# Performance work log

Hardware: AMD Instinct MI355X
Metric: run time of the kernel (lower is better)

## Reference

```python
import jax, jax.numpy as jnp
import numpy as np

B, N, D_IN = 8, 1369, 768
S, D, ITERS = 7, 256, 3
RES, SIGMA = 37, 5.0
EPS = 1e-8


def _ln(x, g, b):
    m = jnp.mean(x, -1, keepdims=True)
    v = jnp.mean((x - m) ** 2, -1, keepdims=True)
    return (x - m) * jax.lax.rsqrt(v + 1e-5) * g + b


def _abs_grid():
    xs = jnp.linspace(-1.0, 1.0, RES)
    ys = jnp.linspace(-1.0, 1.0, RES)
    gx, gy = jnp.meshgrid(xs, ys, indexing='xy')
    return jnp.stack([gx.reshape(-1), gy.reshape(-1)], axis=-1)  # [N,2]


def setup_inputs() -> dict:
    key = jax.random.key(0)
    ks = jax.random.split(key, 40)
    i = iter(range(40))
    def w(shape, scale=0.02):
        return (jax.random.normal(ks[next(i)], shape, jnp.float32) * scale).astype(jnp.float32)
    def zeros(shape):
        return jnp.zeros(shape, jnp.float32)
    xav = float(np.sqrt(6.0 / (S + D)))
    inp = {
        'inputs': jax.random.normal(ks[next(i)], (B, N, D_IN), jnp.float32),
        'slots_init_p': jax.random.uniform(ks[next(i)], (1, S, D), jnp.float32, -xav, xav),
        'S_s0': w((1, S, 1, 2)),
        'S_p0': w((1, S, 1, 2)),
        'im_ln1_g': jnp.ones((D_IN,), jnp.float32), 'im_ln1_b': zeros((D_IN,)),
        'im_w1': w((D_IN, D_IN)), 'im_b1': zeros((D_IN,)),
        'im_w2': w((D_IN, D)), 'im_b2': zeros((D,)),
        'im_ln2_g': jnp.ones((D,), jnp.float32), 'im_ln2_b': zeros((D,)),
        'Wq': w((D, D)), 'Wk': w((D, D)), 'Wv': w((D, D)),
        'g_w': w((2, D)), 'g_b': zeros((D,)),
        'f_w1': w((D, D)), 'f_b1': zeros((D,)),
        'f_w2': w((D, D)), 'f_b2': zeros((D,)),
        'ln_g': jnp.ones((D,), jnp.float32), 'ln_b': zeros((D,)),
        'gru_wih': w((D, 3 * D)), 'gru_whh': w((D, 3 * D)),
        'gru_bih': zeros((3 * D,)), 'gru_bhh': zeros((3 * D,)),
        'mlp_ln_g': jnp.ones((D,), jnp.float32), 'mlp_ln_b': zeros((D,)),
        'mlp_w1': w((D, 4 * D)), 'mlp_b1': zeros((4 * D,)),
        'mlp_w2': w((4 * D, D)), 'mlp_b2': zeros((D,)),
        'fin_w': w((D, D)), 'fin_b': zeros((D,)),
    }
    return inp


def reference(inputs, slots_init_p, S_s0, S_p0,
              im_ln1_g, im_ln1_b, im_w1, im_b1, im_w2, im_b2, im_ln2_g, im_ln2_b,
              Wq, Wk, Wv, g_w, g_b, f_w1, f_b1, f_w2, f_b2,
              ln_g, ln_b, gru_wih, gru_whh, gru_bih, gru_bhh,
              mlp_ln_g, mlp_ln_b, mlp_w1, mlp_b1, mlp_w2, mlp_b2,
              fin_w, fin_b):
    abs_grid = _abs_grid()                    # [N,2], constant buffer
    ag = abs_grid[None, None]                 # [1,1,N,2]
    scale = D ** (-0.5)

    slots = jnp.broadcast_to(slots_init_p, (B, S, D))
    slots_init = slots

    # initial_mlp: LN -> Linear -> ReLU -> Linear -> LN (dropout-free eval path)
    x = _ln(inputs, im_ln1_g, im_ln1_b)
    x = jax.nn.relu(x @ im_w1 + im_b1)
    x = x @ im_w2 + im_b2
    x = _ln(x, im_ln2_g, im_ln2_b)            # [B,N,D]
    KX = x @ Wk                                # slot-independent part of K(inputs)
    VX = x @ Wv

    S_p = jnp.broadcast_to(S_p0, (B, S, 1, 2))
    S_s = jnp.broadcast_to(S_s0, (B, S, 1, 2))

    def f_mlp(z):
        return jax.nn.relu(z @ f_w1 + f_b1) @ f_w2 + f_b2

    attn = None
    slots_prev = slots
    for t in range(ITERS + 1):
        if t == ITERS - 1:  # query_opt straight-through trick
            slots = jax.lax.stop_gradient(slots) + slots_init - jax.lax.stop_gradient(slots_init)
        slots_prev = slots
        sn = _ln(slots, ln_g, ln_b)
        rel = (ag - S_p) / (S_s * SIGMA)      # [B,S,N,2]
        grel = rel @ g_w + g_b                # [B,S,N,D]
        k = f_mlp(KX[:, None] + grel)         # [B,S,N,D]
        v = f_mlp(VX[:, None] + grel)
        q = sn @ Wq                           # [B,S,D]
        dots = jnp.einsum('bsd,bsnd->bsn', q, k) * scale
        attn = jax.nn.softmax(dots, axis=1) + EPS   # softmax over slots
        attn = attn / jnp.sum(attn, -1, keepdims=True)
        updates = jnp.einsum('bsnd,bsn->bsd', v, attn)
        S_p = jnp.einsum('bsn,nd->bsd', attn, abs_grid)[:, :, None, :]
        S_s = jnp.sqrt(jnp.einsum('bsnd,bsn->bsd', (ag - S_p) ** 2, attn))[:, :, None, :]
        if t != ITERS:
            # GRUCell (torch gate order r,z,n)
            gi = updates @ gru_wih + gru_bih
            gh = slots_prev @ gru_whh + gru_bhh
            i_r, i_z, i_n = jnp.split(gi, 3, axis=-1)
            h_r, h_z, h_n = jnp.split(gh, 3, axis=-1)
            r = jax.nn.sigmoid(i_r + h_r)
            z = jax.nn.sigmoid(i_z + h_z)
            n = jnp.tanh(i_n + r * h_n)
            slots = (1.0 - z) * n + z * slots_prev
            # residual pre-norm MLP (dropout identity in eval)
            m = _ln(slots, mlp_ln_g, mlp_ln_b)
            m = jax.nn.relu(m @ mlp_w1 + mlp_b1) @ mlp_w2 + mlp_b2
            slots = slots + m
    out = slots_prev @ fin_w + fin_b
    return out, attn
```

## Files before the change

kernel.cpp:

```cpp
#include <hip/hip_runtime.h>

constexpr int CB   = 8;
constexpr int CN   = 1369;
constexpr int CDIN = 768;
constexpr int CS   = 7;
constexpr int CD   = 256;
constexpr int CITERS = 3;
constexpr int CRES = 37;
constexpr float CSIGMA = 5.0f;
constexpr int CBS = CB * CS;
constexpr int CBN = CB * CN;
constexpr int CKV = 2 * CD;
constexpr float LNEPS = 1e-5f;
constexpr float ATTN_EPS = 1e-8f;

typedef unsigned short u16;
typedef short bs8 __attribute__((ext_vector_type(8)));
typedef float f4 __attribute__((ext_vector_type(4)));

__device__ __forceinline__ float ag_x(int n) { return -1.f + (float)(n % CRES) * (2.f / 36.f); }
__device__ __forceinline__ float ag_y(int n) { return -1.f + (float)(n / CRES) * (2.f / 36.f); }

__device__ __forceinline__ u16 bf_rne(float f) {
    unsigned u = __float_as_uint(f);
    return (u16)((u + 0x7FFFu + ((u >> 16) & 1u)) >> 16);
}
__device__ __forceinline__ float bf_to_f(u16 h) { return __uint_as_float(((unsigned)h) << 16); }

__device__ __forceinline__ void split2b(float v, u16& h, u16& m) {
    h = bf_rne(v);
    m = bf_rne(v - bf_to_f(h));
}

__device__ __forceinline__ void async16(const u16* g, u16* l) {
    __builtin_amdgcn_global_load_lds(
        (const __attribute__((address_space(1))) unsigned int*)g,
        (__attribute__((address_space(3))) unsigned int*)l, 16, 0, 0);
}

__device__ __forceinline__ float block_reduce_sum(float v, float* sbuf) {
    #pragma unroll
    for (int off = 32; off > 0; off >>= 1) v += __shfl_down(v, off, 64);
    if ((threadIdx.x & 63) == 0) sbuf[threadIdx.x >> 6] = v;
    __syncthreads();
    if (threadIdx.x == 0) sbuf[0] = sbuf[0] + sbuf[1] + sbuf[2] + sbuf[3];
    __syncthreads();
    float r = sbuf[0];
    __syncthreads();
    return r;
}

__global__ __launch_bounds__(256) void ln_planes_kernel(const float* __restrict__ in,
        u16* __restrict__ Yh, u16* __restrict__ Ym,
        const float* __restrict__ g, const float* __restrict__ b, int d) {
    __shared__ float sbuf[8];
    int row = blockIdx.x, t = threadIdx.x;
    const float* x = in + (size_t)row * d;
    float v0 = x[t], v1 = 0.f, v2 = 0.f;
    if (d > 256) { v1 = x[t + 256]; v2 = x[t + 512]; }
    float mean = block_reduce_sum(v0 + v1 + v2, sbuf) / d;
    float d0 = v0 - mean, d1 = v1 - mean, d2 = v2 - mean;
    float pv = (d > 256) ? (d0 * d0 + d1 * d1 + d2 * d2) : (d0 * d0);
    float var = block_reduce_sum(pv, sbuf) / d;
    float rstd = rsqrtf(var + LNEPS);
    {
        float y = d0 * rstd * g[t] + b[t];
        u16 h, m; split2b(y, h, m);
        Yh[(size_t)row * d + t] = h; Ym[(size_t)row * d + t] = m;
    }
    if (d > 256) {
        float y1 = d1 * rstd * g[t + 256] + b[t + 256];
        u16 h, m; split2b(y1, h, m);
        Yh[(size_t)row * d + t + 256] = h; Ym[(size_t)row * d + t + 256] = m;
        float y2 = d2 * rstd * g[t + 512] + b[t + 512];
        split2b(y2, h, m);
        Yh[(size_t)row * d + t + 512] = h; Ym[(size_t)row * d + t + 512] = m;
    }
}

__global__ __launch_bounds__(256) void transpose_split2_kernel(const float* __restrict__ W,
        u16* __restrict__ Th, u16* __restrict__ Tm, int K, int N) {
    __shared__ float tile[32][33];
    int nb = blockIdx.x * 32, kb = blockIdx.y * 32;
    int tx = threadIdx.x & 31, ty = threadIdx.x >> 5;
    #pragma unroll
    for (int i = 0; i < 32; i += 8)
        tile[ty + i][tx] = W[(size_t)(kb + ty + i) * N + nb + tx];
    __syncthreads();
    #pragma unroll
    for (int i = 0; i < 32; i += 8) {
        float v = tile[tx][ty + i];
        u16 h, m; split2b(v, h, m);
        size_t idx = (size_t)(nb + ty + i) * K + kb + tx;
        Th[idx] = h; Tm[idx] = m;
    }
}

__global__ __launch_bounds__(256) void wprodT_kernel(const float* __restrict__ A,
        const float* __restrict__ B, u16* __restrict__ Th, u16* __restrict__ Tm) {
    __shared__ float arow[CD];
    int k = blockIdx.x;
    arow[threadIdx.x] = A[k * CD + threadIdx.x];
    __syncthreads();
    int n = threadIdx.x;
    float acc = 0.f;
    for (int j = 0; j < CD; j++) acc += arow[j] * B[(size_t)j * CD + n];
    u16 h, m; split2b(acc, h, m);
    Th[(size_t)n * CD + k] = h;
    Tm[(size_t)n * CD + k] = m;
}

__global__ __launch_bounds__(256) void wprodPq_kernel(const float* __restrict__ Wq,
        const float* __restrict__ f_w2, float* __restrict__ Pq) {
    __shared__ float arow[CD];
    int k = blockIdx.x;
    arow[threadIdx.x] = Wq[k * CD + threadIdx.x];
    __syncthreads();
    int n = threadIdx.x;
    float acc = 0.f;
    for (int c = 0; c < CD; c++) acc += arow[c] * f_w2[(size_t)n * CD + c];
    Pq[(size_t)k * CD + n] = acc;
}

__global__ __launch_bounds__(256) void wprodN_kernel(const float* __restrict__ A,
        const float* __restrict__ B, float* __restrict__ P, int N) {
    __shared__ float arow[CD];
    int k = blockIdx.x;
    arow[threadIdx.x] = A[k * CD + threadIdx.x];
    __syncthreads();
    int n = blockIdx.y * 256 + threadIdx.x;
    if (n >= N) return;
    float acc = 0.f;
    for (int j = 0; j < CD; j++) acc += arow[j] * B[(size_t)j * N + n];
    P[(size_t)k * N + n] = acc;
}

__global__ __launch_bounds__(256) void prep_small_kernel(
        const float* __restrict__ g_w, const float* __restrict__ g_b,
        const float* __restrict__ f_w1, const float* __restrict__ f_b1,
        float* __restrict__ G2, float* __restrict__ gb1,
        const float* __restrict__ f_b2, const float* __restrict__ wih,
        const float* __restrict__ bih, float* __restrict__ bg,
        const float* __restrict__ Wq, float* __restrict__ wqb) {
    int bid = blockIdx.x;
    if (bid == 0) {
        int n = threadIdx.x;
        float a0 = 0.f, a1 = 0.f, ab = 0.f;
        for (int j = 0; j < CD; j++) {
            float w = f_w1[j * CD + n];
            a0 += g_w[j] * w;
            a1 += g_w[CD + j] * w;
            ab += g_b[j] * w;
        }
        G2[n] = a0; G2[CD + n] = a1; gb1[n] = ab + f_b1[n];
    } else if (bid <= 3) {
        int n = (bid - 1) * 256 + threadIdx.x;
        float s = bih[n];
        for (int c = 0; c < CD; c++) s += f_b2[c] * wih[(size_t)c * (3 * CD) + n];
        bg[n] = s;
    } else {
        int j = threadIdx.x;
        float s = 0.f;
        for (int c = 0; c < CD; c++) s += Wq[j * CD + c] * f_b2[c];
        wqb[j] = s;
    }
}

template<int BN, int NBUF>
__global__ __launch_bounds__(256)
void hgemm2(const u16* __restrict__ Ah, const u16* __restrict__ Am,
            const u16* __restrict__ Bh, const u16* __restrict__ Bm,
            int M, int N, int K, const float* __restrict__ bias, int relu,
            float* __restrict__ Cf, u16* __restrict__ Ch, u16* __restrict__ Cm) {
    constexpr int BP = BN * 32;
    constexpr int SB = 4096 + 2 * BP;
    constexpr int NI = 2 + 2 * (BN / 64);
    constexpr int NF = BN / 32;
    constexpr int PP = BN / 64;
    __shared__ u16 smem[NBUF][SB];
    const int tid = threadIdx.x;

    int bx = blockIdx.x, by = blockIdx.y;
    {
        int gx = gridDim.x;
        int nwg = gx * gridDim.y;
        if (!(nwg & 7)) {
            int bid = by * gx + bx;
            int cpx = nwg >> 3;
            int s = (bid & 7) * cpx + (bid >> 3);
            bx = s % gx; by = s / gx;
        }
    }
    const int m0 = by * 64, n0 = bx * BN;
    const int w = tid >> 6, lane = tid & 63;
    const int wm = w & 1, wn = w >> 1;
    const int l15 = lane & 15, l4 = lane >> 4;

    const u16* srcp[NI];
    int dsto[NI];
    #pragma unroll
    for (int i = 0; i < NI; i++) {
        const u16* bp; int row, r, c;
        if (i < 2) {
            int qq = tid;
            r = qq >> 2;
            c = (qq & 3) ^ ((r ^ (r >> 2)) & 3);
            bp = (i == 0) ? Ah : Am;
            row = m0 + r; row = row < M ? row : M - 1;
            dsto[i] = i * 2048 + w * 512;
        } else {
            int ii = i - 2;
            int plane = ii / PP;
            int sub = ii % PP;
            int qq = sub * 256 + tid;
            r = qq >> 2;
            c = (qq & 3) ^ ((r ^ (r >> 2)) & 3);
            bp = plane ? Bm : Bh;
            row = n0 + r;
            dsto[i] = 4096 + plane * BP + sub * 2048 + w * 512;
        }
        srcp[i] = bp + (size_t)row * K + c * 8;
    }

    f4 acc[2][NF];
    #pragma unroll
    for (int i = 0; i < 2; i++)
        #pragma unroll
        for (int j = 0; j < NF; j++) acc[i][j] = (f4){0.f, 0.f, 0.f, 0.f};

    const int cx8 = (l4 ^ (l15 & 3) ^ ((l15 >> 2) & 3)) * 8;

    const int ns = K / 32;
    #pragma unroll
    for (int d = 0; d < NBUF - 1; d++)
        #pragma unroll
        for (int i = 0; i < NI; i++) async16(srcp[i] + d * 32, &smem[d][dsto[i]]);

    u16* c0 = &smem[0][0];
    u16* c1 = &smem[NBUF > 1 ? 1 : 0][0];
    u16* c2 = &smem[NBUF - 1][0];

    for (int k = 0; k < ns; k++) {
        if constexpr (NBUF == 3) {
            if (k + 2 < ns) {
                #pragma unroll
                for (int i = 0; i < NI; i++) async16(srcp[i] + (k + 2) * 32, c2 + dsto[i]);
                if constexpr (BN == 64) asm volatile("s_waitcnt vmcnt(8)" ::: "memory");
                else                     asm volatile("s_waitcnt vmcnt(12)" ::: "memory");
            } else if (k + 1 < ns) {
                if constexpr (BN == 64) asm volatile("s_waitcnt vmcnt(4)" ::: "memory");
                else                     asm volatile("s_waitcnt vmcnt(6)" ::: "memory");
            } else {
                asm volatile("s_waitcnt vmcnt(0)" ::: "memory");
            }
        } else {
            if (k + 1 < ns) {
                #pragma unroll
                for (int i = 0; i < NI; i++) async16(srcp[i] + (k + 1) * 32, c1 + dsto[i]);
                if constexpr (BN == 64) asm volatile("s_waitcnt vmcnt(4)" ::: "memory");
                else                     asm volatile("s_waitcnt vmcnt(6)" ::: "memory");
            } else {
                asm volatile("s_waitcnt vmcnt(0)" ::: "memory");
            }
        }
        __builtin_amdgcn_s_barrier();
        bs8 ah[2], am[2], bh[NF], bm[NF];
        #pragma unroll
        for (int f = 0; f < 2; f++) {
            int oa = (wm * 32 + f * 16 + l15) * 32 + cx8;
            ah[f] = *(const bs8*)(c0 + oa);
            am[f] = *(const bs8*)(c0 + 2048 + oa);
        }
        #pragma unroll
        for (int f = 0; f < NF; f++) {
            int ob = (wn * (NF * 16) + f * 16 + l15) * 32 + cx8;
            bh[f] = *(const bs8*)(c0 + 4096 + ob);
            bm[f] = *(const bs8*)(c0 + 4096 + BP + ob);
        }
        #pragma unroll
        for (int mf = 0; mf < 2; mf++)
            #pragma unroll
            for (int nf = 0; nf < NF; nf++) {
                acc[mf][nf] = __builtin_amdgcn_mfma_f32_16x16x32_bf16(am[mf], bh[nf], acc[mf][nf], 0, 0, 0);
                acc[mf][nf] = __builtin_amdgcn_mfma_f32_16x16x32_bf16(ah[mf], bm[nf], acc[mf][nf], 0, 0, 0);
                acc[mf][nf] = __builtin_amdgcn_mfma_f32_16x16x32_bf16(ah[mf], bh[nf], acc[mf][nf], 0, 0, 0);
            }
        asm volatile("" ::: "memory");
        __builtin_amdgcn_s_barrier();
        if constexpr (NBUF == 3) { u16* t_ = c0; c0 = c1; c1 = c2; c2 = t_; }
        else                     { u16* t_ = c0; c0 = c1; c1 = t_; }
    }

    #pragma unroll
    for (int mf = 0; mf < 2; mf++)
        #pragma unroll
        for (int i = 0; i < 4; i++) {
            int grow = m0 + wm * 32 + mf * 16 + l4 * 4 + i;
            if (grow < M) {
                #pragma unroll
                for (int nf = 0; nf < NF; nf++) {
                    int col = n0 + wn * (NF * 16) + nf * 16 + l15;
                    float v = acc[mf][nf][i] + (bias ? bias[col] : 0.f);
                    if (relu) v = fmaxf(v, 0.f);
                    if (Cf) Cf[(size_t)grow * N + col] = v;
                    else {
                        u16 h, m; split2b(v, h, m);
                        Ch[(size_t)grow * N + col] = h;
                        Cm[(size_t)grow * N + col] = m;
                    }
                }
            }
        }
}

__global__ __launch_bounds__(128) void rowgemm_kernel(const float* __restrict__ A,
        const float* __restrict__ W, const float* __restrict__ bias,
        float* __restrict__ C, int N, int K, int relu,
        const float* __restrict__ resid, const float* __restrict__ resb) {
    __shared__ float sA[1024];
    int r = blockIdx.x;
    int c = blockIdx.y * 128 + threadIdx.x;
    for (int i = threadIdx.x; i < K; i += 128) sA[i] = A[(size_t)r * K + i];
    __syncthreads();
    float a0 = 0.f, a1 = 0.f, a2 = 0.f, a3 = 0.f;
    #pragma unroll 4
    for (int k = 0; k < K; k += 4) {
        a0 += sA[k]     * W[(size_t)k * N + c];
        a1 += sA[k + 1] * W[(size_t)(k + 1) * N + c];
        a2 += sA[k + 2] * W[(size_t)(k + 2) * N + c];
        a3 += sA[k + 3] * W[(size_t)(k + 3) * N + c];
    }
    float v = (a0 + a1) + (a2 + a3) + (bias ? bias[c] : 0.f);
    if (relu) v = fmaxf(v, 0.f);
    if (resid) v += resid[(size_t)r * N + c] + resb[c];
    C[(size_t)r * N + c] = v;
}

__global__ __launch_bounds__(128) void rowgemmG_kernel(
        const float* __restrict__ A0, const float* __restrict__ W0,
        const float* __restrict__ b0, float* __restrict__ C0,
        const float* __restrict__ A1, const float* __restrict__ W1,
        const float* __restrict__ b1, float* __restrict__ C1,
        const float* __restrict__ msum, int N, int K) {
    __shared__ float sA[256];
    const float* A = blockIdx.z ? A1 : A0;
    const float* W = blockIdx.z ? W1 : W0;
    const float* B = blockIdx.z ? b1 : b0;
    float* C = blockIdx.z ? C1 : C0;
    int r = blockIdx.x;
    int c = blockIdx.y * 128 + threadIdx.x;
    float scl = blockIdx.z ? 1.f : 1.f / msum[r * 8];
    for (int i = threadIdx.x; i < K; i += 128) sA[i] = A[(size_t)r * K + i] * scl;
    __syncthreads();
    float a0 = 0.f, a1 = 0.f, a2 = 0.f, a3 = 0.f;
    #pragma unroll 4
    for (int k = 0; k < K; k += 4) {
        a0 += sA[k]     * W[(size_t)k * N + c];
        a1 += sA[k + 1] * W[(size_t)(k + 1) * N + c];
        a2 += sA[k + 2] * W[(size_t)(k + 2) * N + c];
        a3 += sA[k + 3] * W[(size_t)(k + 3) * N + c];
    }
    C[(size_t)r * N + c] = (a0 + a1) + (a2 + a3) + B[c];
}

__global__ __launch_bounds__(256) void init_kernel(const float* __restrict__ slots_init_p,
        const float* __restrict__ S_s0, const float* __restrict__ S_p0,
        float* __restrict__ slots, float* __restrict__ S_s, float* __restrict__ S_p) {
    int bs = blockIdx.x, t = threadIdx.x;
    int s = bs % CS;
    slots[bs * CD + t] = slots_init_p[s * CD + t];
    if (t < 2) { S_s[bs * 2 + t] = S_s0[s * 2 + t]; S_p[bs * 2 + t] = S_p0[s * 2 + t]; }
}

__global__ __launch_bounds__(256) void ln_slots_q_kernel(const float* __restrict__ slots,
        const float* __restrict__ ln_g, const float* __restrict__ ln_b,
        const float* __restrict__ wqb, const float* __restrict__ Pq,
        float* __restrict__ qwb, float* __restrict__ qb0) {
    __shared__ float sbuf[8];
    __shared__ float sN[CD];
    int row = blockIdx.x, t = threadIdx.x;
    float x = slots[row * CD + t];
    float mean = block_reduce_sum(x, sbuf) / CD;
    float d0 = x - mean;
    float var = block_reduce_sum(d0 * d0, sbuf) / CD;
    float sn = d0 * rsqrtf(var + LNEPS) * ln_g[t] + ln_b[t];
    sN[t] = sn;
    float qb = block_reduce_sum(sn * wqb[t], sbuf);
    if (t == 0) qb0[row] = qb;
    __syncthreads();
    float acc = 0.f;
    #pragma unroll 4
    for (int k = 0; k < CD; k++) acc += sN[k] * Pq[(size_t)k * CD + t];
    qwb[row * CD + t] = acc;
}

__global__ __launch_bounds__(256) void dotsv_kernel(const float* __restrict__ KVX,
        const float* __restrict__ S_p, const float* __restrict__ S_s,
        const float* __restrict__ msum_in, int useMsum,
        const float* __restrict__ G2, const float* __restrict__ gb1,
        const float* __restrict__ qw, const float* __restrict__ qb0,
        float* __restrict__ attn, float* __restrict__ Wacc,
        float* __restrict__ msum_out) {
    __shared__ float sred[4 * CD];
    int b = blockIdx.x;
    int w = threadIdx.x >> 6, l = threadIdx.x & 63;
    int k4 = l * 4;
    float4 g0 = *(const float4*)(G2 + k4);
    float4 g1 = *(const float4*)(G2 + CD + k4);
    float4 gb = *(const float4*)(gb1 + k4);
    float4 qwv[CS]; float px[CS], py[CS], ix[CS], iy[CS], q0[CS];
    #pragma unroll
    for (int s = 0; s < CS; s++) {
        int bs = b * CS + s;
        qwv[s] = *(const float4*)(qw + bs * CD + k4);
        if (useMsum) {
            const float* mp = msum_in + bs * 8;
            float m0 = mp[0];
            float pxv = mp[1] / m0, pyv = mp[2] / m0;
            float sx = sqrtf(fmaxf(mp[3] / m0 - pxv * pxv, 0.f));
            float sy = sqrtf(fmaxf(mp[4] / m0 - pyv * pyv, 0.f));
            px[s] = pxv; py[s] = pyv;
            ix[s] = 1.f / (sx * CSIGMA); iy[s] = 1.f / (sy * CSIGMA);
        } else {
            px[s] = S_p[2 * bs]; py[s] = S_p[2 * bs + 1];
            ix[s] = 1.f / (S_s[2 * bs] * CSIGMA); iy[s] = 1.f / (S_s[2 * bs + 1] * CSIGMA);
        }
        q0[s] = qb0[bs];
    }
    float4 acc[CS];
    #pragma unroll
    for (int s = 0; s < CS; s++) acc[s] = make_float4(0.f, 0.f, 0.f, 0.f);
    float wm0[CS], wm1x[CS], wm1y[CS], wm2x[CS], wm2y[CS];
    #pragma unroll
    for (int s = 0; s < CS; s++) { wm0[s] = 0.f; wm1x[s] = 0.f; wm1y[s] = 0.f; wm2x[s] = 0.f; wm2y[s] = 0.f; }
    int nbase = blockIdx.y * 16 + w * 4;
    #pragma unroll
    for (int i = 0; i < 4; i++) {
        int n = nbase + i;
        int nc = n < CN ? n : CN - 1;
        const float* rowp = KVX + (size_t)(b * CN + nc) * CKV;
        float4 kx = *(const float4*)(rowp + k4);
        float ax = ag_x(nc), ay = ag_y(nc);
        float dsv[CS];
        #pragma unroll
        for (int s = 0; s < CS; s++) {
            float r0 = (ax - px[s]) * ix[s];
            float r1 = (ay - py[s]) * iy[s];
            float v0 = fmaxf(kx.x + r0 * g0.x + r1 * g1.x + gb.x, 0.f);
            float v1 = fmaxf(kx.y + r0 * g0.y + r1 * g1.y + gb.y, 0.f);
            float v2 = fmaxf(kx.z + r0 * g0.z + r1 * g1.z + gb.z, 0.f);
            float v3 = fmaxf(kx.w + r0 * g0.w + r1 * g1.w + gb.w, 0.f);
            float d = v0 * qwv[s].x + v1 * qwv[s].y + v2 * qwv[s].z + v3 * qwv[s].w;
            #pragma unroll
            for (int off = 32; off > 0; off >>= 1) d += __shfl_xor(d, off, 64);
            dsv[s] = 0.0625f * (d + q0[s]);
        }
        float mx = -1e30f;
        #pragma unroll
        for (int s = 0; s < CS; s++) mx = fmaxf(mx, dsv[s]);
        float sum = 0.f;
        #pragma unroll
        for (int s = 0; s < CS; s++) { dsv[s] = __expf(dsv[s] - mx); sum += dsv[s]; }
        float inv = 1.f / sum;
        #pragma unroll
        for (int s = 0; s < CS; s++) dsv[s] = dsv[s] * inv + ATTN_EPS;
        if (attn && l == 0 && n < CN) {
            #pragma unroll
            for (int s = 0; s < CS; s++)
                attn[(size_t)(b * CS + s) * CN + n] = dsv[s];
        }
        if (msum_out && n < CN) {
            float ax2 = ax * ax, ay2 = ay * ay;
            #pragma unroll
            for (int s = 0; s < CS; s++) {
                float a = dsv[s];
                wm0[s] += a; wm1x[s] += a * ax; wm1y[s] += a * ay;
                wm2x[s] += a * ax2; wm2y[s] += a * ay2;
            }
        }
        if (Wacc && n < CN) {
            float4 vx = *(const float4*)(rowp + CD + k4);
            #pragma unroll
            for (int s = 0; s < CS; s++) {
                float r0 = (ax - px[s]) * ix[s];
                float r1 = (ay - py[s]) * iy[s];
                float a = dsv[s];
                acc[s].x += a * fmaxf(vx.x + r0 * g0.x + r1 * g1.x + gb.x, 0.f);
                acc[s].y += a * fmaxf(vx.y + r0 * g0.y + r1 * g1.y + gb.y, 0.f);
                acc[s].z += a * fmaxf(vx.z + r0 * g0.z + r1 * g1.z + gb.z, 0.f);
                acc[s].w += a * fmaxf(vx.w + r0 * g0.w + r1 * g1.w + gb.w, 0.f);
            }
        }
    }
    if (Wacc) {
        for (int s = 0; s < CS; s++) {
            ((float4*)sred)[w * 64 + l] = acc[s];
            __syncthreads();
            if (threadIdx.x < CD) {
                float v = sred[threadIdx.x] + sred[CD + threadIdx.x]
                        + sred[2 * CD + threadIdx.x] + sred[3 * CD + threadIdx.x];
                atomicAdd(&Wacc[(size_t)(b * CS + s) * CD + threadIdx.x], v);
            }
            __syncthreads();
        }
    }
    if (msum_out) {
        if (l == 0) {
            #pragma unroll
            for (int s = 0; s < CS; s++) {
                sred[w * 40 + s * 5 + 0] = wm0[s];
                sred[w * 40 + s * 5 + 1] = wm1x[s];
                sred[w * 40 + s * 5 + 2] = wm1y[s];
                sred[w * 40 + s * 5 + 3] = wm2x[s];
                sred[w * 40 + s * 5 + 4] = wm2y[s];
            }
        }
        __syncthreads();
        if (threadIdx.x < 35) {
            int s = threadIdx.x / 5, j = threadIdx.x % 5;
            float v = sred[s * 5 + j] + sred[40 + s * 5 + j]
                    + sred[80 + s * 5 + j] + sred[120 + s * 5 + j];
            atomicAdd(&msum_out[(size_t)(b * CS + s) * 8 + j], v);
        }
    }
}

__global__ __launch_bounds__(256) void attn_moments_kernel(float* __restrict__ u,
        float* __restrict__ S_p, float* __restrict__ S_s, float* __restrict__ inv0,
        int writeNorm) {
    __shared__ float sbuf[8];
    int bs = blockIdx.x;
    float* up = u + (size_t)bs * CN;
    float m0 = 0, m1x = 0, m1y = 0, m2x = 0, m2y = 0;
    for (int n = threadIdx.x; n < CN; n += 256) {
        float uu = up[n];
        float ax = ag_x(n), ay = ag_y(n);
        m0 += uu; m1x += uu * ax; m1y += uu * ay; m2x += uu * ax * ax; m2y += uu * ay * ay;
    }
    m0  = block_reduce_sum(m0, sbuf);
    m1x = block_reduce_sum(m1x, sbuf);
    m1y = block_reduce_sum(m1y, sbuf);
    m2x = block_reduce_sum(m2x, sbuf);
    m2y = block_reduce_sum(m2y, sbuf);
    float px = m1x / m0, py = m1y / m0;
    float inv = 1.f / m0;
    if (threadIdx.x == 0) {
        S_p[2 * bs] = px; S_p[2 * bs + 1] = py;
        S_s[2 * bs]     = sqrtf(fmaxf(m2x / m0 - px * px, 0.f));
        S_s[2 * bs + 1] = sqrtf(fmaxf(m2y / m0 - py * py, 0.f));
        inv0[bs] = inv;
    }
    if (writeNorm)
        for (int n = threadIdx.x; n < CN; n += 256) up[n] = up[n] * inv;
}

__global__ __launch_bounds__(256) void gate_ln_kernel(const float* __restrict__ giRaw,
        const float* __restrict__ ghRaw, const float* __restrict__ slots,
        const float* __restrict__ mg, const float* __restrict__ mb,
        float* __restrict__ snewb, float* __restrict__ sMb,
        float* __restrict__ WaccZ, float* __restrict__ msumZ) {
    __shared__ float sbuf[8];
    int row = blockIdx.x, t = threadIdx.x;
    float gi0 = giRaw[row * 3 * CD + t];
    float gi1 = giRaw[row * 3 * CD + CD + t];
    float gi2 = giRaw[row * 3 * CD + 2 * CD + t];
    float gh0 = ghRaw[row * 3 * CD + t];
    float gh1 = ghRaw[row * 3 * CD + CD + t];
    float gh2 = ghRaw[row * 3 * CD + 2 * CD + t];
    float r = 1.f / (1.f + expf(-(gi0 + gh0)));
    float z = 1.f / (1.f + expf(-(gi1 + gh1)));
    float nn = tanhf(gi2 + r * gh2);
    float snew = (1.f - z) * nn + z * slots[row * CD + t];
    snewb[row * CD + t] = snew;
    WaccZ[row * CD + t] = 0.f;
    if (t < 8) msumZ[row * 8 + t] = 0.f;
    float mean = block_reduce_sum(snew, sbuf) / CD;
    float dv = snew - mean;
    float var = block_reduce_sum(dv * dv, sbuf) / CD;
    sMb[row * CD + t] = dv * rsqrtf(var + LNEPS) * mg[t] + mb[t];
}

extern "C" void kernel_launch(void* const* d_in, const int* in_sizes, int n_in,
                              void* d_out, int out_size, void* d_ws, size_t ws_size,
                              hipStream_t stream) {
    (void)in_sizes; (void)n_in; (void)out_size;
    const float* inputs       = (const float*)d_in[0];
    const float* slots_init_p = (const float*)d_in[1];
    const float* S_s0         = (const float*)d_in[2];
    const float* S_p0         = (const float*)d_in[3];
    const float* im_ln1_g = (const float*)d_in[4];
    const float* im_ln1_b = (const float*)d_in[5];
    const float* im_w1    = (const float*)d_in[6];
    const float* im_b1    = (const float*)d_in[7];
    const float* im_w2    = (const float*)d_in[8];
    const float* im_b2    = (const float*)d_in[9];
    const float* im_ln2_g = (const float*)d_in[10];
    const float* im_ln2_b = (const float*)d_in[11];
    const float* Wq  = (const float*)d_in[12];
    const float* Wk  = (const float*)d_in[13];
    const float* Wv  = (const float*)d_in[14];
    const float* g_w = (const float*)d_in[15];
    const float* g_b = (const float*)d_in[16];
    const float* f_w1 = (const float*)d_in[17];
    const float* f_b1 = (const float*)d_in[18];
    const float* f_w2 = (const float*)d_in[19];
    const float* f_b2 = (const float*)d_in[20];
    const float* ln_g = (const float*)d_in[21];
    const float* ln_b = (const float*)d_in[22];
    const float* gru_wih = (const float*)d_in[23];
    const float* gru_whh = (const float*)d_in[24];
    const float* gru_bih = (const float*)d_in[25];
    const float* gru_bhh = (const float*)d_in[26];
    const float* mlp_ln_g = (const float*)d_in[27];
    const float* mlp_ln_b = (const float*)d_in[28];
    const float* mlp_w1 = (const float*)d_in[29];
    const float* mlp_b1 = (const float*)d_in[30];
    const float* mlp_w2 = (const float*)d_in[31];
    const float* mlp_b2 = (const float*)d_in[32];
    const float* fin_w = (const float*)d_in[33];
    const float* fin_b = (const float*)d_in[34];

    char* base = (char*)d_ws;
    size_t off = 0;
    auto take = [&](size_t bytes) { void* p = base + off; off += (bytes + 255) & ~(size_t)255; return p; };

    float* R1 = (float*)take((size_t)CBN * CDIN * 4);
    float* R2 = (float*)take((size_t)CBN * CDIN * 4);
    u16* w1th = (u16*)take((size_t)CDIN * CDIN * 2);
    u16* w1tm = (u16*)take((size_t)CDIN * CDIN * 2);
    u16* w2th = (u16*)take((size_t)CDIN * CD * 2);
    u16* w2tm = (u16*)take((size_t)CDIN * CD * 2);
    u16* kvth = (u16*)take((size_t)CKV * CD * 2);
    u16* kvtm = (u16*)take((size_t)CKV * CD * 2);
    float* G2b  = (float*)take((size_t)2 * CD * 4);
    float* gb1b = (float*)take((size_t)CD * 4);
    float* Pq   = (float*)take((size_t)CD * CD * 4);
    float* Pg   = (float*)take((size_t)CD * 3 * CD * 4);
    float* bgv  = (float*)take((size_t)3 * CD * 4);
    float* wqbb = (float*)take((size_t)CD * 4);
    float* qwb   = (float*)take((size_t)CBS * CD * 4);
    float* qb0b  = (float*)take((size_t)CBS * 4);
    float* inv0b = (float*)take((size_t)CBS * 4);
    float* Wacc  = (float*)take(((size_t)CBS * CD + 2 * CBS * 8) * 4);
    float* msumA = Wacc + (size_t)CBS * CD;
    float* msumB = msumA + (size_t)CBS * 8;
    float* giRaw = (float*)take((size_t)CBS * 3 * CD * 4);
    float* ghRaw = (float*)take((size_t)CBS * 3 * CD * 4);
    float* snewb = (float*)take((size_t)CBS * CD * 4);
    float* sMb   = (float*)take((size_t)CBS * CD * 4);
    float* h1b   = (float*)take((size_t)CBS * 4 * CD * 4);
    float* S_pA  = (float*)take((size_t)CBS * 2 * 4);
    float* S_sA  = (float*)take((size_t)CBS * 2 * 4);
    float* S_pB  = (float*)take((size_t)CBS * 2 * 4);
    float* S_sB  = (float*)take((size_t)CBS * 2 * 4);
    float* slots = (float*)take((size_t)CBS * CD * 4);
    if (ws_size < off) return;

    float* msum[2] = {msumA, msumB};

    u16* xlnh = (u16*)R1;
    u16* xlnm = xlnh + (size_t)CBN * CDIN;
    u16* X1h  = (u16*)R2;
    u16* X1m  = X1h + (size_t)CBN * CDIN;
    float* xD = R1;
    u16* xDnh = (u16*)(R1 + (size_t)CBN * CD);
    u16* xDnm = xDnh + (size_t)CBN * CD;
    float* KVX = R2;

    float* out0 = (float*)d_out;
    float* attnb = out0 + CBS * CD;

    dim3 blk(256);
    const int gM = (CBN + 63) / 64;
    dim3 gridBN(CB, 86);

    transpose_split2_kernel<<<dim3(CDIN/32, CDIN/32), blk, 0, stream>>>(im_w1, w1th, w1tm, CDIN, CDIN);
    transpose_split2_kernel<<<dim3(CD/32,   CDIN/32), blk, 0, stream>>>(im_w2, w2th, w2tm, CDIN, CD);
    wprodT_kernel<<<dim3(CD), blk, 0, stream>>>(Wk, f_w1, kvth, kvtm);
    wprodT_kernel<<<dim3(CD), blk, 0, stream>>>(Wv, f_w1,
        kvth + (size_t)CD * CD, kvtm + (size_t)CD * CD);
    wprodPq_kernel<<<dim3(CD), blk, 0, stream>>>(Wq, f_w2, Pq);
    wprodN_kernel<<<dim3(CD, 3), blk, 0, stream>>>(f_w2, gru_wih, Pg, 3 * CD);
    prep_small_kernel<<<dim3(5), blk, 0, stream>>>(g_w, g_b, f_w1, f_b1, G2b, gb1b,
        f_b2, gru_wih, gru_bih, bgv, Wq, wqbb);
    hipMemsetAsync(Wacc, 0, ((size_t)CBS * CD + 2 * CBS * 8) * sizeof(float), stream);

    ln_planes_kernel<<<CBN, blk, 0, stream>>>(inputs, xlnh, xlnm, im_ln1_g, im_ln1_b, CDIN);
    hgemm2<128,2><<<dim3(CDIN/128, gM), blk, 0, stream>>>(xlnh, xlnm, w1th, w1tm,
        CBN, CDIN, CDIN, im_b1, 1, nullptr, X1h, X1m);
    hgemm2<64,3><<<dim3(CD/64, gM), blk, 0, stream>>>(X1h, X1m, w2th, w2tm,
        CBN, CD, CDIN, im_b2, 0, xD, nullptr, nullptr);
    ln_planes_kernel<<<CBN, blk, 0, stream>>>(xD, xDnh, xDnm, im_ln2_g, im_ln2_b, CD);
    hgemm2<64,3><<<dim3(CKV/64, gM), blk, 0, stream>>>(xDnh, xDnm, kvth, kvtm,
        CBN, CKV, CD, nullptr, 0, KVX, nullptr, nullptr);
    init_kernel<<<CBS, blk, 0, stream>>>(slots_init_p, S_s0, S_p0, slots, S_sA, S_pA);

    for (int t = 0; t <= CITERS; t++) {
        ln_slots_q_kernel<<<CBS, blk, 0, stream>>>(slots, ln_g, ln_b, wqbb, Pq, qwb, qb0b);
        if (t < CITERS) {
            dotsv_kernel<<<gridBN, blk, 0, stream>>>(KVX, S_pA, S_sA,
                msum[(t + 1) & 1], t > 0 ? 1 : 0, G2b, gb1b,
                qwb, qb0b, nullptr, Wacc, msum[t & 1]);
            rowgemmG_kernel<<<dim3(CBS, 3*CD/128, 2), dim3(128), 0, stream>>>(
                Wacc, Pg, bgv, giRaw, slots, gru_whh, gru_bhh, ghRaw, msum[t & 1], 3 * CD, CD);
            gate_ln_kernel<<<CBS, blk, 0, stream>>>(giRaw, ghRaw, slots,
                mlp_ln_g, mlp_ln_b, snewb, sMb, Wacc, msum[(t + 1) & 1]);
            rowgemm_kernel<<<dim3(CBS, 4*CD/128), dim3(128), 0, stream>>>(sMb, mlp_w1, mlp_b1,
                h1b, 4 * CD, CD, 1, nullptr, nullptr);
            rowgemm_kernel<<<dim3(CBS, CD/128), dim3(128), 0, stream>>>(h1b, mlp_w2, nullptr,
                slots, CD, 4 * CD, 0, snewb, mlp_b2);
        } else {
            dotsv_kernel<<<gridBN, blk, 0, stream>>>(KVX, S_pA, S_sA,
                msum[(t + 1) & 1], 1, G2b, gb1b,
                qwb, qb0b, attnb, nullptr, nullptr);
            attn_moments_kernel<<<CBS, blk, 0, stream>>>(attnb, S_pB, S_sB, inv0b, 1);
        }
    }
    rowgemm_kernel<<<dim3(CBS, CD/128), dim3(128), 0, stream>>>(slots, fin_w, fin_b,
        out0, CD, CD, 0, nullptr, nullptr);
}
```

Baseline: 665.6 us.

## Fuse GRU gate/LN with first MLP layer, merge weight-product kernels, distribute moment accumulation

Merges the three weight-product precompute kernels into one launch. Fuses the GRU gate, layer norm and first MLP matmul into a single kernel that recomputes the gate and LN redundantly in each of 8 column blocks, removing a launch and an intermediate buffer per iteration. In the attention kernel, the per-thread 35-value moment accumulators are replaced by one accumulator per lane selected by lane index, which cuts register pressure and simplifies the shared-memory reduction. The cost is redundant gate/LN work across blocks and some select overhead per point.

```diff
diff --git a/kernel.cpp b/kernel.cpp
--- a/kernel.cpp
+++ b/kernel.cpp
@@ -46,6 +46,16 @@
     if (threadIdx.x == 0) sbuf[0] = sbuf[0] + sbuf[1] + sbuf[2] + sbuf[3];
     __syncthreads();
     float r = sbuf[0];
+    __syncthreads();
+    return r;
+}
+
+__device__ __forceinline__ float block_reduce_sum128(float v, float* sbuf) {
+    #pragma unroll
+    for (int off = 32; off > 0; off >>= 1) v += __shfl_down(v, off, 64);
+    if ((threadIdx.x & 63) == 0) sbuf[threadIdx.x >> 6] = v;
+    __syncthreads();
+    float r = sbuf[0] + sbuf[1];
     __syncthreads();
     return r;
 }
@@ -96,30 +106,33 @@
     }
 }
 
-__global__ __launch_bounds__(256) void wprodT_kernel(const float* __restrict__ A,
-        const float* __restrict__ B, u16* __restrict__ Th, u16* __restrict__ Tm) {
+__global__ __launch_bounds__(256) void wprod3_kernel(
+        const float* __restrict__ Wk, const float* __restrict__ Wv,
+        const float* __restrict__ Wq,
+        const float* __restrict__ f_w1, const float* __restrict__ f_w2,
+        u16* __restrict__ kvth, u16* __restrict__ kvtm, float* __restrict__ Pq) {
     __shared__ float arow[CD];
-    int k = blockIdx.x;
-    arow[threadIdx.x] = A[k * CD + threadIdx.x];
-    __syncthreads();
+    int bid = blockIdx.x;
     int n = threadIdx.x;
-    float acc = 0.f;
-    for (int j = 0; j < CD; j++) acc += arow[j] * B[(size_t)j * CD + n];
-    u16 h, m; split2b(acc, h, m);
-    Th[(size_t)n * CD + k] = h;
-    Tm[(size_t)n * CD + k] = m;
-}
-
-__global__ __launch_bounds__(256) void wprodPq_kernel(const float* __restrict__ Wq,
-        const float* __restrict__ f_w2, float* __restrict__ Pq) {
-    __shared__ float arow[CD];
-    int k = blockIdx.x;
-    arow[threadIdx.x] = Wq[k * CD + threadIdx.x];
-    __syncthreads();
-    int n = threadIdx.x;
-    float acc = 0.f;
-    for (int c = 0; c < CD; c++) acc += arow[c] * f_w2[(size_t)n * CD + c];
-    Pq[(size_t)k * CD + n] = acc;
+    if (bid < 512) {
+        const float* A = (bid < 256) ? Wk : Wv;
+        int k = bid & 255;
+        size_t poff = (bid < 256) ? 0 : (size_t)CD * CD;
+        arow[n] = A[k * CD + n];
+        __syncthreads();
+        float acc = 0.f;
+        for (int j = 0; j < CD; j++) acc += arow[j] * f_w1[(size_t)j * CD + n];
+        u16 h, m; split2b(acc, h, m);
+        kvth[poff + (size_t)n * CD + k] = h;
+        kvtm[poff + (size_t)n * CD + k] = m;
+    } else {
+        int k = bid - 512;
+        arow[n] = Wq[k * CD + n];
+        __syncthreads();
+        float acc = 0.f;
+        for (int c = 0; c < CD; c++) acc += arow[c] * f_w2[(size_t)n * CD + c];
+        Pq[(size_t)k * CD + n] = acc;
+    }
 }
 
 __global__ __launch_bounds__(256) void wprodN_kernel(const float* __restrict__ A,
@@ -430,9 +443,9 @@
     float4 acc[CS];
     #pragma unroll
     for (int s = 0; s < CS; s++) acc[s] = make_float4(0.f, 0.f, 0.f, 0.f);
-    float wm0[CS], wm1x[CS], wm1y[CS], wm2x[CS], wm2y[CS];
-    #pragma unroll
-    for (int s = 0; s < CS; s++) { wm0[s] = 0.f; wm1x[s] = 0.f; wm1y[s] = 0.f; wm2x[s] = 0.f; wm2y[s] = 0.f; }
+    float wmv = 0.f;
+    int sidx = l / 5;
+    int jidx = l - sidx * 5;
     int nbase = blockIdx.y * 16 + w * 4;
     #pragma unroll
     for (int i = 0; i < 4; i++) {
@@ -471,12 +484,19 @@
         }
         if (msum_out && n < CN) {
             float ax2 = ax * ax, ay2 = ay * ay;
-            #pragma unroll
-            for (int s = 0; s < CS; s++) {
-                float a = dsv[s];
-                wm0[s] += a; wm1x[s] += a * ax; wm1y[s] += a * ay;
-                wm2x[s] += a * ax2; wm2y[s] += a * ay2;
-            }
+            float a = dsv[0];
+            a = (sidx == 1) ? dsv[1] : a;
+            a = (sidx == 2) ? dsv[2] : a;
+            a = (sidx == 3) ? dsv[3] : a;
+            a = (sidx == 4) ? dsv[4] : a;
+            a = (sidx == 5) ? dsv[5] : a;
+            a = (sidx == 6) ? dsv[6] : a;
+            float coef = 1.f;
+            coef = (jidx == 1) ? ax : coef;
+            coef = (jidx == 2) ? ay : coef;
+            coef = (jidx == 3) ? ax2 : coef;
+            coef = (jidx == 4) ? ay2 : coef;
+            wmv += a * coef;
         }
         if (Wacc && n < CN) {
             float4 vx = *(const float4*)(rowp + CD + k4);
@@ -505,21 +525,12 @@
         }
     }
     if (msum_out) {
-        if (l == 0) {
-            #pragma unroll
-            for (int s = 0; s < CS; s++) {
-                sred[w * 40 + s * 5 + 0] = wm0[s];
-                sred[w * 40 + s * 5 + 1] = wm1x[s];
-                sred[w * 40 + s * 5 + 2] = wm1y[s];
-                sred[w * 40 + s * 5 + 3] = wm2x[s];
-                sred[w * 40 + s * 5 + 4] = wm2y[s];
-            }
-        }
+        if (l < 35) sred[w * 35 + l] = wmv;
         __syncthreads();
         if (threadIdx.x < 35) {
+            float v = sred[threadIdx.x] + sred[35 + threadIdx.x]
+                    + sred[70 + threadIdx.x] + sred[105 + threadIdx.x];
             int s = threadIdx.x / 5, j = threadIdx.x % 5;
-            float v = sred[s * 5 + j] + sred[40 + s * 5 + j]
-                    + sred[80 + s * 5 + j] + sred[120 + s * 5 + j];
             atomicAdd(&msum_out[(size_t)(b * CS + s) * 8 + j], v);
         }
     }
@@ -554,30 +565,54 @@
         for (int n = threadIdx.x; n < CN; n += 256) up[n] = up[n] * inv;
 }
 
-__global__ __launch_bounds__(256) void gate_ln_kernel(const float* __restrict__ giRaw,
+__global__ __launch_bounds__(128) void gate_mlp1_kernel(const float* __restrict__ giRaw,
         const float* __restrict__ ghRaw, const float* __restrict__ slots,
         const float* __restrict__ mg, const float* __restrict__ mb,
-        float* __restrict__ snewb, float* __restrict__ sMb,
+        const float* __restrict__ mlp_w1, const float* __restrict__ mlp_b1,
+        float* __restrict__ snewb, float* __restrict__ h1b,
         float* __restrict__ WaccZ, float* __restrict__ msumZ) {
-    __shared__ float sbuf[8];
+    __shared__ float sbuf[4];
+    __shared__ float sM[CD];
     int row = blockIdx.x, t = threadIdx.x;
-    float gi0 = giRaw[row * 3 * CD + t];
-    float gi1 = giRaw[row * 3 * CD + CD + t];
-    float gi2 = giRaw[row * 3 * CD + 2 * CD + t];
-    float gh0 = ghRaw[row * 3 * CD + t];
-    float gh1 = ghRaw[row * 3 * CD + CD + t];
-    float gh2 = ghRaw[row * 3 * CD + 2 * CD + t];
-    float r = 1.f / (1.f + expf(-(gi0 + gh0)));
-    float z = 1.f / (1.f + expf(-(gi1 + gh1)));
-    float nn = tanhf(gi2 + r * gh2);
-    float snew = (1.f - z) * nn + z * slots[row * CD + t];
-    snewb[row * CD + t] = snew;
-    WaccZ[row * CD + t] = 0.f;
-    if (t < 8) msumZ[row * 8 + t] = 0.f;
-    float mean = block_reduce_sum(snew, sbuf) / CD;
-    float dv = snew - mean;
-    float var = block_reduce_sum(dv * dv, sbuf) / CD;
-    sMb[row * CD + t] = dv * rsqrtf(var + LNEPS) * mg[t] + mb[t];
+    float snew[2];
+    #pragma unroll
+    for (int e = 0; e < 2; e++) {
+        int tt = t + e * 128;
+        float gi0 = giRaw[row * 3 * CD + tt];
+        float gi1 = giRaw[row * 3 * CD + CD + tt];
+        float gi2 = giRaw[row * 3 * CD + 2 * CD + tt];
+        float gh0 = ghRaw[row * 3 * CD + tt];
+        float gh1 = ghRaw[row * 3 * CD + CD + tt];
+        float gh2 = ghRaw[row * 3 * CD + 2 * CD + tt];
+        float r = 1.f / (1.f + expf(-(gi0 + gh0)));
+        float z = 1.f / (1.f + expf(-(gi1 + gh1)));
+        float nn = tanhf(gi2 + r * gh2);
+        snew[e] = (1.f - z) * nn + z * slots[row * CD + tt];
+    }
+    if (blockIdx.y == 0) {
+        snewb[row * CD + t] = snew[0];
+        snewb[row * CD + t + 128] = snew[1];
+        WaccZ[row * CD + t] = 0.f;
+        WaccZ[row * CD + t + 128] = 0.f;
+        if (t < 8) msumZ[row * 8 + t] = 0.f;
+    }
+    float mean = block_reduce_sum128(snew[0] + snew[1], sbuf) / CD;
+    float d0 = snew[0] - mean, d1 = snew[1] - mean;
+    float var = block_reduce_sum128(d0 * d0 + d1 * d1, sbuf) / CD;
+    float rstd = rsqrtf(var + LNEPS);
+    sM[t]       = d0 * rstd * mg[t] + mb[t];
+    sM[t + 128] = d1 * rstd * mg[t + 128] + mb[t + 128];
+    __syncthreads();
+    int c = blockIdx.y * 128 + t;
+    float a0 = 0.f, a1 = 0.f, a2 = 0.f, a3 = 0.f;
+    #pragma unroll 4
+    for (int k = 0; k < CD; k += 4) {
+        a0 += sM[k]     * mlp_w1[(size_t)k * (4 * CD) + c];
+        a1 += sM[k + 1] * mlp_w1[(size_t)(k + 1) * (4 * CD) + c];
+        a2 += sM[k + 2] * mlp_w1[(size_t)(k + 2) * (4 * CD) + c];
+        a3 += sM[k + 3] * mlp_w1[(size_t)(k + 3) * (4 * CD) + c];
+    }
+    h1b[(size_t)row * (4 * CD) + c] = fmaxf((a0 + a1) + (a2 + a3) + mlp_b1[c], 0.f);
 }
 
 extern "C" void kernel_launch(void* const* d_in, const int* in_sizes, int n_in,
@@ -647,10 +682,7 @@
     float* giRaw = (float*)take((size_t)CBS * 3 * CD * 4);
     float* ghRaw = (float*)take((size_t)CBS * 3 * CD * 4);
     float* snewb = (float*)take((size_t)CBS * CD * 4);
-    float* sMb   = (float*)take((size_t)CBS * CD * 4);
     float* h1b   = (float*)take((size_t)CBS * 4 * CD * 4);
-    float* S_pA  = (float*)take((size_t)CBS * 2 * 4);
-    float* S_sA  = (float*)take((size_t)CBS * 2 * 4);
     float* S_pB  = (float*)take((size_t)CBS * 2 * 4);
     float* S_sB  = (float*)take((size_t)CBS * 2 * 4);
     float* slots = (float*)take((size_t)CBS * CD * 4);
@@ -676,10 +708,7 @@
 
     transpose_split2_kernel<<<dim3(CDIN/32, CDIN/32), blk, 0, stream>>>(im_w1, w1th, w1tm, CDIN, CDIN);
     transpose_split2_kernel<<<dim3(CD/32,   CDIN/32), blk, 0, stream>>>(im_w2, w2th, w2tm, CDIN, CD);
-    wprodT_kernel<<<dim3(CD), blk, 0, stream>>>(Wk, f_w1, kvth, kvtm);
-    wprodT_kernel<<<dim3(CD), blk, 0, stream>>>(Wv, f_w1,
-        kvth + (size_t)CD * CD, kvtm + (size_t)CD * CD);
-    wprodPq_kernel<<<dim3(CD), blk, 0, stream>>>(Wq, f_w2, Pq);
+    wprod3_kernel<<<dim3(768), blk, 0, stream>>>(Wk, Wv, Wq, f_w1, f_w2, kvth, kvtm, Pq);
     wprodN_kernel<<<dim3(CD, 3), blk, 0, stream>>>(f_w2, gru_wih, Pg, 3 * CD);
     prep_small_kernel<<<dim3(5), blk, 0, stream>>>(g_w, g_b, f_w1, f_b1, G2b, gb1b,
         f_b2, gru_wih, gru_bih, bgv, Wq, wqbb);
@@ -693,24 +722,22 @@
     ln_planes_kernel<<<CBN, blk, 0, stream>>>(xD, xDnh, xDnm, im_ln2_g, im_ln2_b, CD);
     hgemm2<64,3><<<dim3(CKV/64, gM), blk, 0, stream>>>(xDnh, xDnm, kvth, kvtm,
         CBN, CKV, CD, nullptr, 0, KVX, nullptr, nullptr);
-    init_kernel<<<CBS, blk, 0, stream>>>(slots_init_p, S_s0, S_p0, slots, S_sA, S_pA);
+    init_kernel<<<CBS, blk, 0, stream>>>(slots_init_p, S_s0, S_p0, slots, S_sB, S_pB);
 
     for (int t = 0; t <= CITERS; t++) {
         ln_slots_q_kernel<<<CBS, blk, 0, stream>>>(slots, ln_g, ln_b, wqbb, Pq, qwb, qb0b);
         if (t < CITERS) {
-            dotsv_kernel<<<gridBN, blk, 0, stream>>>(KVX, S_pA, S_sA,
+            dotsv_kernel<<<gridBN, blk, 0, stream>>>(KVX, S_pB, S_sB,
                 msum[(t + 1) & 1], t > 0 ? 1 : 0, G2b, gb1b,
                 qwb, qb0b, nullptr, Wacc, msum[t & 1]);
             rowgemmG_kernel<<<dim3(CBS, 3*CD/128, 2), dim3(128), 0, stream>>>(
                 Wacc, Pg, bgv, giRaw, slots, gru_whh, gru_bhh, ghRaw, msum[t & 1], 3 * CD, CD);
-            gate_ln_kernel<<<CBS, blk, 0, stream>>>(giRaw, ghRaw, slots,
-                mlp_ln_g, mlp_ln_b, snewb, sMb, Wacc, msum[(t + 1) & 1]);
-            rowgemm_kernel<<<dim3(CBS, 4*CD/128), dim3(128), 0, stream>>>(sMb, mlp_w1, mlp_b1,
-                h1b, 4 * CD, CD, 1, nullptr, nullptr);
+            gate_mlp1_kernel<<<dim3(CBS, 8), dim3(128), 0, stream>>>(giRaw, ghRaw, slots,
+                mlp_ln_g, mlp_ln_b, mlp_w1, mlp_b1, snewb, h1b, Wacc, msum[(t + 1) & 1]);
             rowgemm_kernel<<<dim3(CBS, CD/128), dim3(128), 0, stream>>>(h1b, mlp_w2, nullptr,
                 slots, CD, 4 * CD, 0, snewb, mlp_b2);
         } else {
-            dotsv_kernel<<<gridBN, blk, 0, stream>>>(KVX, S_pA, S_sA,
+            dotsv_kernel<<<gridBN, blk, 0, stream>>>(KVX, S_pB, S_sB,
                 msum[(t + 1) & 1], 1, G2b, gb1b,
                 qwb, qb0b, attnb, nullptr, nullptr);
             attn_moments_kernel<<<CBS, blk, 0, stream>>>(attnb, S_pB, S_sB, inv0b, 1);
```

Measured after the change: 647.3 us. 1.03x faster.
